# Performance work log

Measured on AMD Instinct MI355X. Metric: run time of the kernel, lower is better.

## Reference

```python
import jax, jax.numpy as jnp
import numpy as np

B = 1024        # number of graphs in batch
NNODES = 64     # nodes per graph
NODE = 4        # node feature size
EDGEF = 2       # edge feature size
HID = 32        # hidden_dim
NFACT = 3       # num_factories
NE = 1024       # edges per graph (self.edges list length)


def setup_inputs() -> dict:
    key = jax.random.key(0)
    ks = jax.random.split(key, 12)
    rng = np.random.default_rng(1)
    # per-graph edge list (self.edges in the torch module)
    edges = rng.integers(0, NNODES, size=(NE, 2))
    edges_src = jnp.asarray(edges[:, 0], dtype=jnp.int32)   # [NE]
    edges_dst = jnp.asarray(edges[:, 1], dtype=jnp.int32)   # [NE]
    # batched edge_index for EdgeConv: same per-graph edges offset by b*NNODES
    offs = np.arange(B, dtype=np.int64)[:, None] * NNODES   # [B,1]
    ei_src = (edges[:, 0][None, :] + offs).reshape(-1)
    ei_dst = (edges[:, 1][None, :] + offs).reshape(-1)
    edge_index = jnp.asarray(np.stack([ei_src, ei_dst], 0), dtype=jnp.int32)  # [2, B*NE]

    N = B * NNODES
    E = B * NE
    x = jax.random.normal(ks[0], (N, NODE), dtype=jnp.float32)
    edge_attr = jax.random.normal(ks[1], (E, EDGEF), dtype=jnp.float32)
    action = jax.random.uniform(ks[2], (B, NE + NFACT), dtype=jnp.float32)

    s = 0.1
    W1 = jax.random.normal(ks[3], (2 * NODE + EDGEF, HID), dtype=jnp.float32) * s
    b1 = jnp.zeros((HID,), jnp.float32)
    W2 = jax.random.normal(ks[4], (HID, HID), dtype=jnp.float32) * s
    b2 = jnp.zeros((HID,), jnp.float32)
    D = (NODE + HID) * 2 + 1  # 73
    Wl = jax.random.normal(ks[5], (D, HID), dtype=jnp.float32) * s
    bl = jnp.zeros((HID,), jnp.float32)
    Wv = jax.random.normal(ks[6], (HID, 1), dtype=jnp.float32) * s
    bv = jnp.zeros((1,), jnp.float32)

    return {"x": x, "edge_index": edge_index, "edge_attr": edge_attr,
            "action": action, "edges_src": edges_src, "edges_dst": edges_dst,
            "W1": W1, "b1": b1, "W2": W2, "b2": b2,
            "Wl": Wl, "bl": bl, "Wv": Wv, "bv": bv}


def reference(x, edge_index, edge_attr, action, edges_src, edges_dst,
              W1, b1, W2, b2, Wl, bl, Wv, bv):
    N = x.shape[0]
    src = edge_index[0]  # flow='target_to_source': x_i = x[src], aggregate at src
    dst = edge_index[1]
    # EdgeConv message: MLP(cat[x_i, x_j, edge_attr])
    tmp = jnp.concatenate([x[src], x[dst], edge_attr], axis=1)  # [E, 10]
    msg = jax.nn.relu(tmp @ W1 + b1) @ W2 + b2                  # [E, HID]
    x_pp = jax.ops.segment_sum(msg, src, num_segments=N)        # scatter-add
    # concat node feats with conv output, split into graphs
    h = jnp.concatenate([x, x_pp], axis=1).reshape(B, NNODES, NODE + HID)  # [B,NN,36]
    # gather per-edge endpoint features
    ef = jnp.concatenate([h[:, edges_src], h[:, edges_dst]], axis=2)       # [B,NE,72]
    # factory features: last NFACT nodes duplicated
    pf = jnp.concatenate([h[:, -NFACT:], h[:, -NFACT:]], axis=-1)          # [B,NF,72]
    feats = jnp.concatenate([ef, pf], axis=1)                               # [B,NE+NF,72]
    concat = jnp.concatenate([feats, action[..., None]], axis=-1)           # [B,NE+NF,73]
    hidden = jax.nn.relu(concat @ Wl + bl)                                  # [B,NE+NF,HID]
    v = hidden @ Wv + bv                                                    # [B,NE+NF,1]
    return jnp.sum(v, axis=1).squeeze(-1)                                   # [B]
```

## Files before the change

### kernel.cpp

```cpp
#include <hip/hip_runtime.h>

#define NNODES 64
#define HID 32
#define NFACT 3
#define NE 1024
#define NROWS (NE + NFACT)
#define TPB 512
#define STR 36
#define QSTRH 20
#define MAXTILES 128
#define EPT (NE / TPB)

typedef short bf16x8 __attribute__((ext_vector_type(8)));
typedef float f32x4  __attribute__((ext_vector_type(4)));
typedef float f32x16 __attribute__((ext_vector_type(16)));

__device__ __forceinline__ unsigned pack_bf2(float lo, float hi) {
    unsigned ul = __builtin_bit_cast(unsigned, lo);
    unsigned uh = __builtin_bit_cast(unsigned, hi);
    ul += 0x7fffu + ((ul >> 16) & 1u);
    uh += 0x7fffu + ((uh >> 16) & 1u);
    return (ul >> 16) | (uh & 0xffff0000u);
}
__device__ __forceinline__ short f2bf(float f) {
    unsigned u = __builtin_bit_cast(unsigned, f);
    u += 0x7fffu + ((u >> 16) & 1u);
    return (short)(u >> 16);
}
__device__ __forceinline__ float bflo(unsigned u) { return __builtin_bit_cast(float, u << 16); }
__device__ __forceinline__ float bfhi(unsigned u) { return __builtin_bit_cast(float, u & 0xffff0000u); }
__device__ __forceinline__ float4 fma4(float a, float4 w, float4 c) {
    c.x = fmaf(a, w.x, c.x); c.y = fmaf(a, w.y, c.y);
    c.z = fmaf(a, w.z, c.z); c.w = fmaf(a, w.w, c.w);
    return c;
}

__global__ __launch_bounds__(TPB, 6) void critic_fused(
    const float* __restrict__ x,
    const float* __restrict__ edge_attr,
    const float* __restrict__ action,
    const int*   __restrict__ es,
    const int*   __restrict__ ed,
    const float* __restrict__ W1,
    const float* __restrict__ b1,
    const float* __restrict__ W2,
    const float* __restrict__ b2,
    const float* __restrict__ Wl,
    const float* __restrict__ bl,
    const float* __restrict__ Wv,
    const float* __restrict__ bv,
    float* __restrict__ out)
{
    const int b    = blockIdx.x;
    const int tid  = threadIdx.x;
    const int lane = tid & 63;
    const int wv   = tid >> 6;
    const int quad = lane >> 4;
    const int m16  = lane & 15;
    const int kh   = quad * 8;

    __shared__ __align__(16) float4 xs4[NNODES];
    __shared__ __align__(16) float  xpp[NNODES * STR];
    __shared__ __align__(16) float  qp0[NNODES * STR];
    __shared__ __align__(16) float  qp1[NNODES * STR];
    __shared__ __align__(16) float  W1s[10 * HID];
    __shared__ float  b1s[HID];
    __shared__ float  wred[TPB / 64];
    __shared__ int    sdeg[NNODES], soff[NNODES], scnt[NNODES];
    __shared__ int    tns[MAXTILES];
    __shared__ int    pep[MAXTILES * 16];
    __shared__ int    snt;

    unsigned* qh0 = (unsigned*)qp0;
    unsigned* qh1 = (unsigned*)qp1;

    if (tid < NNODES) { xs4[tid] = ((const float4*)x)[b * NNODES + tid]; sdeg[tid] = 0; scnt[tid] = 0; }
    if (tid < 80) ((float4*)W1s)[tid] = ((const float4*)W1)[tid];
    if (tid < HID) b1s[tid] = b1[tid];
    if (tid < MAXTILES) tns[tid] = 0;
#pragma unroll
    for (int i = 0; i < MAXTILES * 16 / TPB; i++) pep[tid + i * TPB] = 0xFFF;
    {
        const float4 z4 = make_float4(0.f, 0.f, 0.f, 0.f);
#pragma unroll 1
        for (int i = tid; i < NNODES * STR / 4; i += TPB) ((float4*)xpp)[i] = z4;
    }

    int ces[EPT], ced[EPT];
#pragma unroll
    for (int i = 0; i < EPT; i++) {
        ces[i] = es[tid + i * TPB];
        ced[i] = ed[tid + i * TPB];
    }
    __syncthreads();

#pragma unroll
    for (int i = 0; i < EPT; i++) atomicAdd(&sdeg[ces[i]], 1);
    {
        const int  n  = lane;
        const int  k0 = (wv & 3) * 8;
        const bool g1 = (wv < 4);
        const int  rb = g1 ? 0 : 4;
        const float4 xv = xs4[n];
        float4 qa, qb;
        if (g1) {
            const float4* b1v = (const float4*)&b1s[k0];
            qa = b1v[0]; qb = b1v[1];
        } else {
            qa = make_float4(0.f, 0.f, 0.f, 0.f); qb = qa;
        }
#pragma unroll 1
        for (int i = 0; i < 4; i++) {
            const float xi = (i == 0) ? xv.x : (i == 1) ? xv.y : (i == 2) ? xv.z : xv.w;
            const float4* wa = (const float4*)&W1s[(rb + i) * HID + k0];
            qa = fma4(xi, wa[0], qa); qb = fma4(xi, wa[1], qb);
        }
        uint4 p;
        p.x = pack_bf2(qa.x, qa.y); p.y = pack_bf2(qa.z, qa.w);
        p.z = pack_bf2(qb.x, qb.y); p.w = pack_bf2(qb.z, qb.w);
        unsigned* dst = g1 ? qh0 : qh1;
        *(uint4*)&dst[n * QSTRH + (wv & 3) * 4] = p;
    }
    __syncthreads();

    if (tid < NNODES) {
        const int cnt = (sdeg[tid] + 15) >> 4;
        int scan = cnt;
#pragma unroll
        for (int o = 1; o < 64; o <<= 1) {
            const int v = __shfl_up(scan, o);
            if (tid >= o) scan += v;
        }
        const int base = scan - cnt;
        soff[tid] = base;
        if (tid == NNODES - 1) snt = scan;
#pragma unroll 1
        for (int j = 0; j < cnt; j++) tns[base + j] = tid;
    }
    __syncthreads();

#pragma unroll
    for (int i = 0; i < EPT; i++) {
        const int n = ces[i];
        const int idx = atomicAdd(&scnt[n], 1);
        pep[soff[n] * 16 + idx] = (tid + i * TPB) | (ced[i] << 12) | (n << 18);
    }
    __syncthreads();

    {
        const float2* ea2 = (const float2*)edge_attr + (size_t)b * NE;
        const int NW   = TPB / 64;
        const int klo  = (lane >> 5) * 8;
        const int klo2 = klo >> 1;
        const int n32  = lane & 31;

        const float4* w8l = (const float4*)&W1s[8 * HID + klo];
        const float4* w8h = (const float4*)&W1s[8 * HID + 16 + klo];
        const float4* w9l = (const float4*)&W1s[9 * HID + klo];
        const float4* w9h = (const float4*)&W1s[9 * HID + 16 + klo];
        const float4 w8a = w8l[0], w8b = w8l[1], w8c = w8h[0], w8d = w8h[1];
        const float4 w9a = w9l[0], w9b = w9l[1], w9c = w9h[0], w9d = w9h[1];

        bf16x8 bfA, bfB;
#pragma unroll
        for (int j = 0; j < 8; j++) {
            bfA[j] = f2bf(W2[(klo + j) * HID + n32]);
            bfB[j] = f2bf(W2[(16 + klo + j) * HID + n32]);
        }

        const int np = (snt + 1) >> 1;

#pragma unroll 1
        for (int p = wv; p < np; p += NW) {
            const int raw = pep[p * 32 + n32];
            const int tA  = tns[2 * p];
            const int tB  = tns[2 * p + 1];
            const int e    = raw & 0xFFF;
            const bool pad = (e == 0xFFF);
            const int d0   = (raw >> 12) & 63;
            const int nd   = (raw >> 18) & 63;
            const float2 ea = ea2[pad ? 0 : e];

            const uint4 A1 = *(const uint4*)&qh0[nd * QSTRH + klo2];
            const uint4 A2 = *(const uint4*)&qh0[nd * QSTRH + 8 + klo2];
            const uint4 G1 = *(const uint4*)&qh1[d0 * QSTRH + klo2];
            const uint4 G2 = *(const uint4*)&qh1[d0 * QSTRH + 8 + klo2];

            const float hx0 = fmaxf(bflo(A1.x) + bflo(G1.x) + ea.x * w8a.x + ea.y * w9a.x, 0.f);
            const float hx1 = fmaxf(bfhi(A1.x) + bfhi(G1.x) + ea.x * w8a.y + ea.y * w9a.y, 0.f);
            const float hx2 = fmaxf(bflo(A1.y) + bflo(G1.y) + ea.x * w8a.z + ea.y * w9a.z, 0.f);
            const float hx3 = fmaxf(bfhi(A1.y) + bfhi(G1.y) + ea.x * w8a.w + ea.y * w9a.w, 0.f);
            const float hx4 = fmaxf(bflo(A1.z) + bflo(G1.z) + ea.x * w8b.x + ea.y * w9b.x, 0.f);
            const float hx5 = fmaxf(bfhi(A1.z) + bfhi(G1.z) + ea.x * w8b.y + ea.y * w9b.y, 0.f);
            const float hx6 = fmaxf(bflo(A1.w) + bflo(G1.w) + ea.x * w8b.z + ea.y * w9b.z, 0.f);
            const float hx7 = fmaxf(bfhi(A1.w) + bfhi(G1.w) + ea.x * w8b.w + ea.y * w9b.w, 0.f);
            const float hy0 = fmaxf(bflo(A2.x) + bflo(G2.x) + ea.x * w8c.x + ea.y * w9c.x, 0.f);
            const float hy1 = fmaxf(bfhi(A2.x) + bfhi(G2.x) + ea.x * w8c.y + ea.y * w9c.y, 0.f);
            const float hy2 = fmaxf(bflo(A2.y) + bflo(G2.y) + ea.x * w8c.z + ea.y * w9c.z, 0.f);
            const float hy3 = fmaxf(bfhi(A2.y) + bfhi(G2.y) + ea.x * w8c.w + ea.y * w9c.w, 0.f);
            const float hy4 = fmaxf(bflo(A2.z) + bflo(G2.z) + ea.x * w8d.x + ea.y * w9d.x, 0.f);
            const float hy5 = fmaxf(bfhi(A2.z) + bfhi(G2.z) + ea.x * w8d.y + ea.y * w9d.y, 0.f);
            const float hy6 = fmaxf(bflo(A2.w) + bflo(G2.w) + ea.x * w8d.z + ea.y * w9d.z, 0.f);
            const float hy7 = fmaxf(bfhi(A2.w) + bfhi(G2.w) + ea.x * w8d.w + ea.y * w9d.w, 0.f);

            uint4 pkA, pkB;
            pkA.x = pad ? 0u : pack_bf2(hx0, hx1);
            pkA.y = pad ? 0u : pack_bf2(hx2, hx3);
            pkA.z = pad ? 0u : pack_bf2(hx4, hx5);
            pkA.w = pad ? 0u : pack_bf2(hx6, hx7);
            pkB.x = pad ? 0u : pack_bf2(hy0, hy1);
            pkB.y = pad ? 0u : pack_bf2(hy2, hy3);
            pkB.z = pad ? 0u : pack_bf2(hy4, hy5);
            pkB.w = pad ? 0u : pack_bf2(hy6, hy7);
            const bf16x8 afA = __builtin_bit_cast(bf16x8, pkA);
            const bf16x8 afB = __builtin_bit_cast(bf16x8, pkB);

            f32x16 c;
#pragma unroll
            for (int j = 0; j < 16; j++) c[j] = 0.0f;
            c = __builtin_amdgcn_mfma_f32_32x32x16_bf16(afA, bfA, c, 0, 0, 0);
            c = __builtin_amdgcn_mfma_f32_32x32x16_bf16(afB, bfB, c, 0, 0, 0);

            float sA = ((c[0] + c[1]) + (c[2] + c[3])) + ((c[4] + c[5]) + (c[6] + c[7]));
            float sB = ((c[8] + c[9]) + (c[10] + c[11])) + ((c[12] + c[13]) + (c[14] + c[15]));
            sA += __shfl_xor(sA, 32);
            sB += __shfl_xor(sB, 32);
            const int   nst = (lane < 32) ? tA : tB;
            const float sv  = (lane < 32) ? sA : sB;
            atomicAdd(&xpp[nst * STR + n32], sv);
        }
    }
    __syncthreads();

    const bool g1p   = (wv < 4);
    const int  cbase = g1p ? 4 : 40;
    const int  xbase = g1p ? 0 : 36;
    bf16x8 bPa, bPb;
#pragma unroll
    for (int j = 0; j < 8; j++) {
        bPa[j] = f2bf(Wl[(cbase + kh + j) * HID + m16]);
        bPb[j] = f2bf(Wl[(cbase + kh + j) * HID + 16 + m16]);
    }
    float wxa[4], wxb[4];
#pragma unroll
    for (int i = 0; i < 4; i++) {
        wxa[i] = Wl[(xbase + i) * HID + m16];
        wxb[i] = Wl[(xbase + i) * HID + 16 + m16];
    }
    const float bca = g1p ? bl[m16] : 0.f;
    const float bcb = g1p ? bl[16 + m16] : 0.f;
    float b2k[8];
#pragma unroll
    for (int j = 0; j < 8; j++) b2k[j] = b2[kh + j];
    const int   mrow = (wv & 3) * 16 + m16;
    const float dn   = (float)sdeg[mrow];

    {
        const float4* xr = (const float4*)&xpp[mrow * STR + kh];
        float4 x0 = xr[0], x1 = xr[1];
        x0.x = fmaf(dn, b2k[0], x0.x); x0.y = fmaf(dn, b2k[1], x0.y);
        x0.z = fmaf(dn, b2k[2], x0.z); x0.w = fmaf(dn, b2k[3], x0.w);
        x1.x = fmaf(dn, b2k[4], x1.x); x1.y = fmaf(dn, b2k[5], x1.y);
        x1.z = fmaf(dn, b2k[6], x1.z); x1.w = fmaf(dn, b2k[7], x1.w);
        uint4 packed;
        packed.x = pack_bf2(x0.x, x0.y);
        packed.y = pack_bf2(x0.z, x0.w);
        packed.z = pack_bf2(x1.x, x1.y);
        packed.w = pack_bf2(x1.z, x1.w);
        const bf16x8 af = __builtin_bit_cast(bf16x8, packed);

        f32x4 ca, cb;
#pragma unroll
        for (int r = 0; r < 4; r++) {
            const float4 xv = xs4[(wv & 3) * 16 + quad * 4 + r];
            float a0 = bca, a1 = bcb;
#pragma unroll
            for (int i = 0; i < 4; i++) {
                const float xi = (i == 0) ? xv.x : (i == 1) ? xv.y : (i == 2) ? xv.z : xv.w;
                a0 = fmaf(xi, wxa[i], a0);
                a1 = fmaf(xi, wxb[i], a1);
            }
            ca[r] = a0; cb[r] = a1;
        }
        ca = __builtin_amdgcn_mfma_f32_16x16x32_bf16(af, bPa, ca, 0, 0, 0);
        cb = __builtin_amdgcn_mfma_f32_16x16x32_bf16(af, bPb, cb, 0, 0, 0);

        __syncthreads();
        float* dst = g1p ? qp0 : qp1;
#pragma unroll
        for (int r = 0; r < 4; r++) {
            const int row = (wv & 3) * 16 + quad * 4 + r;
            dst[row * STR + m16]      = ca[r];
            dst[row * STR + 16 + m16] = cb[r];
        }
    }
    __syncthreads();

    float vsum = 0.0f;
    {
        const float* actb = action + (size_t)b * NROWS;
        const float bvv = bv[0];
        const float* Wl72 = Wl + 72 * HID;
#pragma unroll 1
        for (int i = 0; i < EPT; i++) {
            const int na = ces[i], nb = ced[i];
            const float a = actb[tid + i * TPB];
            const float4* p1v = (const float4*)&qp0[na * STR];
            const float4* p2v = (const float4*)&qp1[nb * STR];
            float v0 = bvv, v1 = 0.0f;
#pragma unroll 1
            for (int q = 0; q < 8; q += 2) {
                const float4 pa0 = p1v[q],     pb0 = p2v[q];
                const float4 pa1 = p1v[q + 1], pb1 = p2v[q + 1];
                const int k = q * 4;
                v0 += fmaxf(pa0.x + pb0.x + a * Wl72[k+0], 0.f) * Wv[k+0];
                v1 += fmaxf(pa0.y + pb0.y + a * Wl72[k+1], 0.f) * Wv[k+1];
                v0 += fmaxf(pa0.z + pb0.z + a * Wl72[k+2], 0.f) * Wv[k+2];
                v1 += fmaxf(pa0.w + pb0.w + a * Wl72[k+3], 0.f) * Wv[k+3];
                v0 += fmaxf(pa1.x + pb1.x + a * Wl72[k+4], 0.f) * Wv[k+4];
                v1 += fmaxf(pa1.y + pb1.y + a * Wl72[k+5], 0.f) * Wv[k+5];
                v0 += fmaxf(pa1.z + pb1.z + a * Wl72[k+6], 0.f) * Wv[k+6];
                v1 += fmaxf(pa1.w + pb1.w + a * Wl72[k+7], 0.f) * Wv[k+7];
            }
            vsum += v0 + v1;
        }
        if (tid < NFACT) {
            const int r = NE + tid;
            const int na = NNODES - NFACT + tid;
            const float a = actb[r];
            const float4* p1v = (const float4*)&qp0[na * STR];
            const float4* p2v = (const float4*)&qp1[na * STR];
            float v = bvv;
#pragma unroll 1
            for (int q = 0; q < 8; q++) {
                const float4 pa = p1v[q], pb = p2v[q];
                const int k = q * 4;
                v += fmaxf(pa.x + pb.x + a * Wl72[k+0], 0.f) * Wv[k+0];
                v += fmaxf(pa.y + pb.y + a * Wl72[k+1], 0.f) * Wv[k+1];
                v += fmaxf(pa.z + pb.z + a * Wl72[k+2], 0.f) * Wv[k+2];
                v += fmaxf(pa.w + pb.w + a * Wl72[k+3], 0.f) * Wv[k+3];
            }
            vsum += v;
        }
    }

#pragma unroll
    for (int off = 32; off > 0; off >>= 1)
        vsum += __shfl_down(vsum, off, 64);
    if ((tid & 63) == 0) wred[tid >> 6] = vsum;
    __syncthreads();
    if (tid == 0) {
        float t = 0.0f;
#pragma unroll
        for (int w = 0; w < TPB / 64; w++) t += wred[w];
        out[b] = t;
    }
}

extern "C" void kernel_launch(void* const* d_in, const int* in_sizes, int n_in,
                              void* d_out, int out_size, void* d_ws, size_t ws_size,
                              hipStream_t stream) {
    const float* x         = (const float*)d_in[0];
    const float* edge_attr = (const float*)d_in[2];
    const float* action    = (const float*)d_in[3];
    const int*   es        = (const int*)d_in[4];
    const int*   ed        = (const int*)d_in[5];
    const float* W1        = (const float*)d_in[6];
    const float* b1        = (const float*)d_in[7];
    const float* W2        = (const float*)d_in[8];
    const float* b2        = (const float*)d_in[9];
    const float* Wl        = (const float*)d_in[10];
    const float* bl        = (const float*)d_in[11];
    const float* Wv        = (const float*)d_in[12];
    const float* bv        = (const float*)d_in[13];
    float* out = (float*)d_out;

    critic_fused<<<dim3(out_size), dim3(TPB), 0, stream>>>(
        x, edge_attr, action, es, ed, W1, b1, W2, b2, Wl, bl, Wv, bv, out);
}
```

Measured before the change: 128.4 us.

## Switch edge-MLP and readout math to packed fp16 with f16 MFMA

Converts the per-edge first-layer activations from bf16 with scalar fp32 math to packed fp16 arithmetic (packed add, fma, max), and switches the second-layer MFMA to the f16 variant. The readout stage now stores the per-node projections as packed fp16 pairs, which halves their LDS footprint. Each readout row is evaluated with packed fp16 ops plus fdot2 accumulation instead of scalar fp32 loops. This is meant to cut VALU instruction count and LDS traffic, at the cost of fp16 range and precision (round-toward-zero packing) in intermediate activations.

```diff
diff --git a/kernel.cpp b/kernel.cpp
--- a/kernel.cpp
+++ b/kernel.cpp
@@ -14,6 +14,8 @@
 typedef short bf16x8 __attribute__((ext_vector_type(8)));
 typedef float f32x4  __attribute__((ext_vector_type(4)));
 typedef float f32x16 __attribute__((ext_vector_type(16)));
+typedef _Float16 f16x2 __attribute__((ext_vector_type(2)));
+typedef _Float16 f16x8 __attribute__((ext_vector_type(8)));
 
 __device__ __forceinline__ unsigned pack_bf2(float lo, float hi) {
     unsigned ul = __builtin_bit_cast(unsigned, lo);
@@ -27,8 +29,19 @@
     u += 0x7fffu + ((u >> 16) & 1u);
     return (short)(u >> 16);
 }
-__device__ __forceinline__ float bflo(unsigned u) { return __builtin_bit_cast(float, u << 16); }
-__device__ __forceinline__ float bfhi(unsigned u) { return __builtin_bit_cast(float, u & 0xffff0000u); }
+__device__ __forceinline__ f16x2 pkrtz(float lo, float hi) {
+    return __builtin_bit_cast(f16x2, __builtin_amdgcn_cvt_pkrtz(lo, hi));
+}
+__device__ __forceinline__ f16x2 packh2_rne(float lo, float hi) {
+    f16x2 r; r.x = (_Float16)lo; r.y = (_Float16)hi; return r;
+}
+__device__ __forceinline__ float dot2acc(f16x2 a, f16x2 b, float c) {
+#if __has_builtin(__builtin_amdgcn_fdot2)
+    return __builtin_amdgcn_fdot2(a, b, c, false);
+#else
+    return c + (float)a.x * (float)b.x + (float)a.y * (float)b.y;
+#endif
+}
 __device__ __forceinline__ float4 fma4(float a, float4 w, float4 c) {
     c.x = fmaf(a, w.x, c.x); c.y = fmaf(a, w.y, c.y);
     c.z = fmaf(a, w.z, c.z); c.w = fmaf(a, w.w, c.w);
@@ -58,6 +71,7 @@
     const int quad = lane >> 4;
     const int m16  = lane & 15;
     const int kh   = quad * 8;
+    const f16x2 z2 = { (_Float16)0.f, (_Float16)0.f };
 
     __shared__ __align__(16) float4 xs4[NNODES];
     __shared__ __align__(16) float  xpp[NNODES * STR];
@@ -116,8 +130,10 @@
             qa = fma4(xi, wa[0], qa); qb = fma4(xi, wa[1], qb);
         }
         uint4 p;
-        p.x = pack_bf2(qa.x, qa.y); p.y = pack_bf2(qa.z, qa.w);
-        p.z = pack_bf2(qb.x, qb.y); p.w = pack_bf2(qb.z, qb.w);
+        p.x = __builtin_bit_cast(unsigned, pkrtz(qa.x, qa.y));
+        p.y = __builtin_bit_cast(unsigned, pkrtz(qa.z, qa.w));
+        p.z = __builtin_bit_cast(unsigned, pkrtz(qb.x, qb.y));
+        p.w = __builtin_bit_cast(unsigned, pkrtz(qb.z, qb.w));
         unsigned* dst = g1 ? qh0 : qh1;
         *(uint4*)&dst[n * QSTRH + (wv & 3) * 4] = p;
     }
@@ -154,18 +170,19 @@
         const int klo2 = klo >> 1;
         const int n32  = lane & 31;
 
-        const float4* w8l = (const float4*)&W1s[8 * HID + klo];
-        const float4* w8h = (const float4*)&W1s[8 * HID + 16 + klo];
-        const float4* w9l = (const float4*)&W1s[9 * HID + klo];
-        const float4* w9h = (const float4*)&W1s[9 * HID + 16 + klo];
-        const float4 w8a = w8l[0], w8b = w8l[1], w8c = w8h[0], w8d = w8h[1];
-        const float4 w9a = w9l[0], w9b = w9l[1], w9c = w9h[0], w9d = w9h[1];
-
-        bf16x8 bfA, bfB;
+        f16x2 w8p[4], w8q[4], w9p[4], w9q[4];
+#pragma unroll
+        for (int j = 0; j < 4; j++) {
+            w8p[j] = packh2_rne(W1s[8 * HID + klo + 2 * j],      W1s[8 * HID + klo + 2 * j + 1]);
+            w8q[j] = packh2_rne(W1s[8 * HID + 16 + klo + 2 * j], W1s[8 * HID + 16 + klo + 2 * j + 1]);
+            w9p[j] = packh2_rne(W1s[9 * HID + klo + 2 * j],      W1s[9 * HID + klo + 2 * j + 1]);
+            w9q[j] = packh2_rne(W1s[9 * HID + 16 + klo + 2 * j], W1s[9 * HID + 16 + klo + 2 * j + 1]);
+        }
+        f16x8 hfA, hfB;
 #pragma unroll
         for (int j = 0; j < 8; j++) {
-            bfA[j] = f2bf(W2[(klo + j) * HID + n32]);
-            bfB[j] = f2bf(W2[(16 + klo + j) * HID + n32]);
+            hfA[j] = (_Float16)W2[(klo + j) * HID + n32];
+            hfB[j] = (_Float16)W2[(16 + klo + j) * HID + n32];
         }
 
         const int np = (snt + 1) >> 1;
@@ -186,40 +203,34 @@
             const uint4 G1 = *(const uint4*)&qh1[d0 * QSTRH + klo2];
             const uint4 G2 = *(const uint4*)&qh1[d0 * QSTRH + 8 + klo2];
 
-            const float hx0 = fmaxf(bflo(A1.x) + bflo(G1.x) + ea.x * w8a.x + ea.y * w9a.x, 0.f);
-            const float hx1 = fmaxf(bfhi(A1.x) + bfhi(G1.x) + ea.x * w8a.y + ea.y * w9a.y, 0.f);
-            const float hx2 = fmaxf(bflo(A1.y) + bflo(G1.y) + ea.x * w8a.z + ea.y * w9a.z, 0.f);
-            const float hx3 = fmaxf(bfhi(A1.y) + bfhi(G1.y) + ea.x * w8a.w + ea.y * w9a.w, 0.f);
-            const float hx4 = fmaxf(bflo(A1.z) + bflo(G1.z) + ea.x * w8b.x + ea.y * w9b.x, 0.f);
-            const float hx5 = fmaxf(bfhi(A1.z) + bfhi(G1.z) + ea.x * w8b.y + ea.y * w9b.y, 0.f);
-            const float hx6 = fmaxf(bflo(A1.w) + bflo(G1.w) + ea.x * w8b.z + ea.y * w9b.z, 0.f);
-            const float hx7 = fmaxf(bfhi(A1.w) + bfhi(G1.w) + ea.x * w8b.w + ea.y * w9b.w, 0.f);
-            const float hy0 = fmaxf(bflo(A2.x) + bflo(G2.x) + ea.x * w8c.x + ea.y * w9c.x, 0.f);
-            const float hy1 = fmaxf(bfhi(A2.x) + bfhi(G2.x) + ea.x * w8c.y + ea.y * w9c.y, 0.f);
-            const float hy2 = fmaxf(bflo(A2.y) + bflo(G2.y) + ea.x * w8c.z + ea.y * w9c.z, 0.f);
-            const float hy3 = fmaxf(bfhi(A2.y) + bfhi(G2.y) + ea.x * w8c.w + ea.y * w9c.w, 0.f);
-            const float hy4 = fmaxf(bflo(A2.z) + bflo(G2.z) + ea.x * w8d.x + ea.y * w9d.x, 0.f);
-            const float hy5 = fmaxf(bfhi(A2.z) + bfhi(G2.z) + ea.x * w8d.y + ea.y * w9d.y, 0.f);
-            const float hy6 = fmaxf(bflo(A2.w) + bflo(G2.w) + ea.x * w8d.z + ea.y * w9d.z, 0.f);
-            const float hy7 = fmaxf(bfhi(A2.w) + bfhi(G2.w) + ea.x * w8d.w + ea.y * w9d.w, 0.f);
-
-            uint4 pkA, pkB;
-            pkA.x = pad ? 0u : pack_bf2(hx0, hx1);
-            pkA.y = pad ? 0u : pack_bf2(hx2, hx3);
-            pkA.z = pad ? 0u : pack_bf2(hx4, hx5);
-            pkA.w = pad ? 0u : pack_bf2(hx6, hx7);
-            pkB.x = pad ? 0u : pack_bf2(hy0, hy1);
-            pkB.y = pad ? 0u : pack_bf2(hy2, hy3);
-            pkB.z = pad ? 0u : pack_bf2(hy4, hy5);
-            pkB.w = pad ? 0u : pack_bf2(hy6, hy7);
-            const bf16x8 afA = __builtin_bit_cast(bf16x8, pkA);
-            const bf16x8 afB = __builtin_bit_cast(bf16x8, pkB);
+            const f16x2 ex2 = pkrtz(ea.x, ea.x);
+            const f16x2 ey2 = pkrtz(ea.y, ea.y);
+            const unsigned pz = pad ? 0u : 0xFFFFFFFFu;
+
+            uint4 pa4, pb4;
+#define MSLOT(dst, au, gu, w8, w9) { \
+            f16x2 t = __builtin_bit_cast(f16x2, au) + __builtin_bit_cast(f16x2, gu); \
+            t = __builtin_elementwise_fma(ex2, w8, t); \
+            t = __builtin_elementwise_fma(ey2, w9, t); \
+            t = __builtin_elementwise_max(t, z2); \
+            dst = __builtin_bit_cast(unsigned, t) & pz; }
+            MSLOT(pa4.x, A1.x, G1.x, w8p[0], w9p[0])
+            MSLOT(pa4.y, A1.y, G1.y, w8p[1], w9p[1])
+            MSLOT(pa4.z, A1.z, G1.z, w8p[2], w9p[2])
+            MSLOT(pa4.w, A1.w, G1.w, w8p[3], w9p[3])
+            MSLOT(pb4.x, A2.x, G2.x, w8q[0], w9q[0])
+            MSLOT(pb4.y, A2.y, G2.y, w8q[1], w9q[1])
+            MSLOT(pb4.z, A2.z, G2.z, w8q[2], w9q[2])
+            MSLOT(pb4.w, A2.w, G2.w, w8q[3], w9q[3])
+#undef MSLOT
+            const f16x8 afA = __builtin_bit_cast(f16x8, pa4);
+            const f16x8 afB = __builtin_bit_cast(f16x8, pb4);
 
             f32x16 c;
 #pragma unroll
             for (int j = 0; j < 16; j++) c[j] = 0.0f;
-            c = __builtin_amdgcn_mfma_f32_32x32x16_bf16(afA, bfA, c, 0, 0, 0);
-            c = __builtin_amdgcn_mfma_f32_32x32x16_bf16(afB, bfB, c, 0, 0, 0);
+            c = __builtin_amdgcn_mfma_f32_32x32x16_f16(afA, hfA, c, 0, 0, 0);
+            c = __builtin_amdgcn_mfma_f32_32x32x16_f16(afB, hfB, c, 0, 0, 0);
 
             float sA = ((c[0] + c[1]) + (c[2] + c[3])) + ((c[4] + c[5]) + (c[6] + c[7]));
             float sB = ((c[8] + c[9]) + (c[10] + c[11])) + ((c[12] + c[13]) + (c[14] + c[15]));
@@ -286,12 +297,11 @@
         cb = __builtin_amdgcn_mfma_f32_16x16x32_bf16(af, bPb, cb, 0, 0, 0);
 
         __syncthreads();
-        float* dst = g1p ? qp0 : qp1;
+        unsigned* dsth = g1p ? qh0 : qh1;
 #pragma unroll
         for (int r = 0; r < 4; r++) {
             const int row = (wv & 3) * 16 + quad * 4 + r;
-            dst[row * STR + m16]      = ca[r];
-            dst[row * STR + 16 + m16] = cb[r];
+            dsth[row * QSTRH + m16] = __builtin_bit_cast(unsigned, pkrtz(ca[r], cb[r]));
         }
     }
     __syncthreads();
@@ -301,47 +311,72 @@
         const float* actb = action + (size_t)b * NROWS;
         const float bvv = bv[0];
         const float* Wl72 = Wl + 72 * HID;
+        f16x2 wlh[16], wvh[16];
+#pragma unroll
+        for (int j = 0; j < 16; j++) {
+            wlh[j] = packh2_rne(Wl72[j], Wl72[j + 16]);
+            wvh[j] = packh2_rne(Wv[j],  Wv[j + 16]);
+        }
+
+#define CSLOT(j, pu, qu, acc) { \
+        f16x2 t = __builtin_bit_cast(f16x2, pu) + __builtin_bit_cast(f16x2, qu); \
+        t = __builtin_elementwise_fma(a2, wlh[j], t); \
+        t = __builtin_elementwise_max(t, z2); \
+        acc = dot2acc(t, wvh[j], acc); }
+
 #pragma unroll 1
         for (int i = 0; i < EPT; i++) {
             const int na = ces[i], nb = ced[i];
             const float a = actb[tid + i * TPB];
-            const float4* p1v = (const float4*)&qp0[na * STR];
-            const float4* p2v = (const float4*)&qp1[nb * STR];
+            const unsigned* ra = &qh0[na * QSTRH];
+            const unsigned* rb = &qh1[nb * QSTRH];
+            const uint4 Pa0 = *(const uint4*)&ra[0];
+            const uint4 Pa1 = *(const uint4*)&ra[4];
+            const uint4 Pa2 = *(const uint4*)&ra[8];
+            const uint4 Pa3 = *(const uint4*)&ra[12];
+            const uint4 Pb0 = *(const uint4*)&rb[0];
+            const uint4 Pb1 = *(const uint4*)&rb[4];
+            const uint4 Pb2 = *(const uint4*)&rb[8];
+            const uint4 Pb3 = *(const uint4*)&rb[12];
+            const f16x2 a2 = pkrtz(a, a);
             float v0 = bvv, v1 = 0.0f;
-#pragma unroll 1
-            for (int q = 0; q < 8; q += 2) {
-                const float4 pa0 = p1v[q],     pb0 = p2v[q];
-                const float4 pa1 = p1v[q + 1], pb1 = p2v[q + 1];
-                const int k = q * 4;
-                v0 += fmaxf(pa0.x + pb0.x + a * Wl72[k+0], 0.f) * Wv[k+0];
-                v1 += fmaxf(pa0.y + pb0.y + a * Wl72[k+1], 0.f) * Wv[k+1];
-                v0 += fmaxf(pa0.z + pb0.z + a * Wl72[k+2], 0.f) * Wv[k+2];
-                v1 += fmaxf(pa0.w + pb0.w + a * Wl72[k+3], 0.f) * Wv[k+3];
-                v0 += fmaxf(pa1.x + pb1.x + a * Wl72[k+4], 0.f) * Wv[k+4];
-                v1 += fmaxf(pa1.y + pb1.y + a * Wl72[k+5], 0.f) * Wv[k+5];
-                v0 += fmaxf(pa1.z + pb1.z + a * Wl72[k+6], 0.f) * Wv[k+6];
-                v1 += fmaxf(pa1.w + pb1.w + a * Wl72[k+7], 0.f) * Wv[k+7];
-            }
+            CSLOT( 0, Pa0.x, Pb0.x, v0) CSLOT( 1, Pa0.y, Pb0.y, v1)
+            CSLOT( 2, Pa0.z, Pb0.z, v0) CSLOT( 3, Pa0.w, Pb0.w, v1)
+            CSLOT( 4, Pa1.x, Pb1.x, v0) CSLOT( 5, Pa1.y, Pb1.y, v1)
+            CSLOT( 6, Pa1.z, Pb1.z, v0) CSLOT( 7, Pa1.w, Pb1.w, v1)
+            CSLOT( 8, Pa2.x, Pb2.x, v0) CSLOT( 9, Pa2.y, Pb2.y, v1)
+            CSLOT(10, Pa2.z, Pb2.z, v0) CSLOT(11, Pa2.w, Pb2.w, v1)
+            CSLOT(12, Pa3.x, Pb3.x, v0) CSLOT(13, Pa3.y, Pb3.y, v1)
+            CSLOT(14, Pa3.z, Pb3.z, v0) CSLOT(15, Pa3.w, Pb3.w, v1)
             vsum += v0 + v1;
         }
         if (tid < NFACT) {
             const int r = NE + tid;
             const int na = NNODES - NFACT + tid;
             const float a = actb[r];
-            const float4* p1v = (const float4*)&qp0[na * STR];
-            const float4* p2v = (const float4*)&qp1[na * STR];
-            float v = bvv;
-#pragma unroll 1
-            for (int q = 0; q < 8; q++) {
-                const float4 pa = p1v[q], pb = p2v[q];
-                const int k = q * 4;
-                v += fmaxf(pa.x + pb.x + a * Wl72[k+0], 0.f) * Wv[k+0];
-                v += fmaxf(pa.y + pb.y + a * Wl72[k+1], 0.f) * Wv[k+1];
-                v += fmaxf(pa.z + pb.z + a * Wl72[k+2], 0.f) * Wv[k+2];
-                v += fmaxf(pa.w + pb.w + a * Wl72[k+3], 0.f) * Wv[k+3];
-            }
-            vsum += v;
-        }
+            const unsigned* ra = &qh0[na * QSTRH];
+            const unsigned* rb = &qh1[na * QSTRH];
+            const uint4 Pa0 = *(const uint4*)&ra[0];
+            const uint4 Pa1 = *(const uint4*)&ra[4];
+            const uint4 Pa2 = *(const uint4*)&ra[8];
+            const uint4 Pa3 = *(const uint4*)&ra[12];
+            const uint4 Pb0 = *(const uint4*)&rb[0];
+            const uint4 Pb1 = *(const uint4*)&rb[4];
+            const uint4 Pb2 = *(const uint4*)&rb[8];
+            const uint4 Pb3 = *(const uint4*)&rb[12];
+            const f16x2 a2 = pkrtz(a, a);
+            float v0 = bvv, v1 = 0.0f;
+            CSLOT( 0, Pa0.x, Pb0.x, v0) CSLOT( 1, Pa0.y, Pb0.y, v1)
+            CSLOT( 2, Pa0.z, Pb0.z, v0) CSLOT( 3, Pa0.w, Pb0.w, v1)
+            CSLOT( 4, Pa1.x, Pb1.x, v0) CSLOT( 5, Pa1.y, Pb1.y, v1)
+            CSLOT( 6, Pa1.z, Pb1.z, v0) CSLOT( 7, Pa1.w, Pb1.w, v1)
+            CSLOT( 8, Pa2.x, Pb2.x, v0) CSLOT( 9, Pa2.y, Pb2.y, v1)
+            CSLOT(10, Pa2.z, Pb2.z, v0) CSLOT(11, Pa2.w, Pb2.w, v1)
+            CSLOT(12, Pa3.x, Pb3.x, v0) CSLOT(13, Pa3.y, Pb3.y, v1)
+            CSLOT(14, Pa3.z, Pb3.z, v0) CSLOT(15, Pa3.w, Pb3.w, v1)
+            vsum += v0 + v1;
+        }
+#undef CSLOT
     }
 
 #pragma unroll
```

Measured after the change: 122.0 us. 5.0% less time.
